# Kernel tuning notes

Hardware: AMD Instinct MI355X
Metric: run time of the kernel (lower is better)

Reference implementation:

```python
import jax, jax.numpy as jnp
import numpy as np

N_NODES = 50000
IN_DIM = 128
HIDDEN = 64
OUT_DIM = 3
HEADS1 = 4
NEG_SLOPE = 0.2
EPS = 1e-16


def _glorot(key, shape):
    fan_in, fan_out = shape[0], shape[-1]
    lim = (6.0 / (fan_in + fan_out)) ** 0.5
    return jax.random.uniform(key, shape, jnp.float32, -lim, lim)


def setup_inputs() -> dict:
    key = jax.random.key(0)
    ks = jax.random.split(key, 12)
    x = jax.random.normal(ks[0], (N_NODES, IN_DIM), jnp.float32)
    edge_index = jax.random.randint(ks[1], (2, 400000), 0, N_NODES, jnp.int64)
    # layer 1: GATConv(in=128, out=64, heads=4)
    W1 = _glorot(ks[2], (IN_DIM, HEADS1 * HIDDEN))
    att_src1 = _glorot(ks[3], (HEADS1, HIDDEN))
    att_dst1 = _glorot(ks[4], (HEADS1, HIDDEN))
    b1 = jnp.zeros((HEADS1 * HIDDEN,), jnp.float32)
    # layer 2: GATConv(in=256, out=64, heads=1)
    W2 = _glorot(ks[5], (HEADS1 * HIDDEN, HIDDEN))
    att_src2 = _glorot(ks[6], (1, HIDDEN))
    att_dst2 = _glorot(ks[7], (1, HIDDEN))
    b2 = jnp.zeros((HIDDEN,), jnp.float32)
    # output linear
    Wout = _glorot(ks[8], (HIDDEN, OUT_DIM))
    bout = jnp.zeros((OUT_DIM,), jnp.float32)
    return {"x": x, "edge_index": edge_index, "W1": W1, "att_src1": att_src1,
            "att_dst1": att_dst1, "b1": b1, "W2": W2, "att_src2": att_src2,
            "att_dst2": att_dst2, "b2": b2, "Wout": Wout, "bout": bout}


def gat_conv(x, src, dst, W, a_src, a_dst, b, n_nodes):
    H, C = a_src.shape
    h = (x @ W).reshape(n_nodes, H, C)            # [N,H,C]
    a_s = jnp.sum(h * a_src[None], axis=-1)        # [N,H]
    a_d = jnp.sum(h * a_dst[None], axis=-1)        # [N,H]
    e = jax.nn.leaky_relu(a_s[src] + a_d[dst], NEG_SLOPE)  # [E,H]
    # segment softmax over incoming edges of each dst node
    m = jax.ops.segment_max(e, dst, num_segments=n_nodes)
    ex = jnp.exp(e - m[dst])
    denom = jax.ops.segment_sum(ex, dst, num_segments=n_nodes)
    alpha = ex / (denom[dst] + EPS)                # [E,H]
    msg = h[src] * alpha[..., None]                # [E,H,C]
    out = jax.ops.segment_sum(msg, dst, num_segments=n_nodes)
    return out.reshape(n_nodes, H * C) + b


def reference(x, edge_index, W1, att_src1, att_dst1, b1, W2, att_src2, att_dst2, b2, Wout, bout):
    n = x.shape[0]
    loop = jnp.arange(n, dtype=edge_index.dtype)
    src = jnp.concatenate([edge_index[0], loop])   # add self loops (PyG default)
    dst = jnp.concatenate([edge_index[1], loop])
    h = gat_conv(x, src, dst, W1, att_src1, att_dst1, b1, n)
    h = jax.nn.elu(h)
    h = gat_conv(h, src, dst, W2, att_src2, att_dst2, b2, n)
    h = jax.nn.elu(h)
    return h @ Wout + bout
```

## Files before the change

kernel.cpp:

```cpp
#include <hip/hip_runtime.h>
#include <hip/hip_bf16.h>
#include <math.h>

#define N_NODES  50000
#define IN_DIM   128
#define HIDDEN   64
#define OUT_DIM  3
#define HEADS1   4
#define E_RAW    400000
#define E_TOT    450000
#define NEG_SLOPE 0.2f
#define SCAN_CHUNK 1024
#define N_CHUNKS ((N_NODES + SCAN_CHUNK - 1) / SCAN_CHUNK)
#define WPREP_BLOCKS 128

typedef __attribute__((ext_vector_type(8))) short bf16x8;
typedef __attribute__((ext_vector_type(4))) float f32x4;

static __device__ __forceinline__ float bfu(unsigned short u) {
    return __uint_as_float(((unsigned)u) << 16);
}
static __device__ __forceinline__ unsigned short f2b_bits(float v) {
    __hip_bfloat16 b = __float2bfloat16(v);
    return *reinterpret_cast<unsigned short*>(&b);
}

static __device__ __forceinline__ void get_edge(const int* __restrict__ ei, int is64,
                                                int e, int& s, int& d) {
    if (e >= E_RAW) { s = d = e - E_RAW; return; }
    if (is64) { s = ei[2 * e]; d = ei[2 * E_RAW + 2 * e]; }
    else      { s = ei[e];     d = ei[E_RAW + e]; }
    s = min(max(s, 0), N_NODES - 1);
    d = min(max(d, 0), N_NODES - 1);
}

__global__ void detect_zero_kernel(const int* __restrict__ ei, int* __restrict__ flag,
                                   int* __restrict__ deg) {
    int gid = blockIdx.x * 256 + threadIdx.x;
    for (int i = gid; i < N_NODES; i += 64 * 256) deg[i] = 0;
    if (blockIdx.x == 0) {
        int nz = 0;
        #pragma unroll 4
        for (int t = 0; t < 32; t++) {
            int i = t * 256 + threadIdx.x;
            nz |= ei[2 * i + 1];
        }
        __shared__ int s;
        if (threadIdx.x == 0) s = 0;
        __syncthreads();
        if (__any(nz != 0) && (threadIdx.x & 63) == 0) s = 1;
        __syncthreads();
        if (threadIdx.x == 0) flag[0] = s ? 0 : 1;
    }
}

__global__ void wprep_count_kernel(const float* __restrict__ W1, __hip_bfloat16* __restrict__ W1T,
                                   const float* __restrict__ W2, __hip_bfloat16* __restrict__ W2T,
                                   const int* __restrict__ ei, const int* __restrict__ flag,
                                   int* __restrict__ deg) {
    int bid = blockIdx.x;
    if (bid < WPREP_BLOCKS) {
        int i = bid * 256 + threadIdx.x;
        if (i < 256 * 128) {
            int n = i >> 7, k = i & 127;
            *((unsigned short*)W1T + i) = f2b_bits(W1[k * 256 + n]);
        }
        if (i < 64 * 256) {
            int n = i >> 8, k = i & 255;
            *((unsigned short*)W2T + i) = f2b_bits(W2[k * 64 + n]);
        }
        return;
    }
    int e = (bid - WPREP_BLOCKS) * 256 + threadIdx.x;
    if (e >= E_TOT) return;
    int s, d;
    get_edge(ei, flag[0], e, s, d);
    atomicAdd(&deg[d], 1);
}

__global__ void scan_local_kernel(const int* __restrict__ deg, int* __restrict__ row_ptr,
                                  int* __restrict__ bsums) {
    __shared__ int wsum[4];
    int t = threadIdx.x;
    int wv = t >> 6, ln = t & 63;
    int g = blockIdx.x * 256 + t;
    int4 d = (g < 12500) ? ((const int4*)deg)[g] : make_int4(0, 0, 0, 0);
    int p0 = d.x, p1 = p0 + d.y, p2 = p1 + d.z, p3 = p2 + d.w;
    int s = p3;
    #pragma unroll
    for (int off = 1; off < 64; off <<= 1) {
        int u = __shfl_up(s, off, 64);
        if (ln >= off) s += u;
    }
    if (ln == 63) wsum[wv] = s;
    __syncthreads();
    int wbase = 0;
    #pragma unroll
    for (int w = 0; w < 4; w++) wbase += (w < wv) ? wsum[w] : 0;
    int ex = wbase + s - p3;
    if (g < 12500) {
        int i = g * 4;
        row_ptr[i + 1] = ex + p0;
        row_ptr[i + 2] = ex + p1;
        row_ptr[i + 3] = ex + p2;
        row_ptr[i + 4] = ex + p3;
    }
    if (t == 255) bsums[blockIdx.x] = wbase + s;
    if (blockIdx.x == 0 && t == 0) row_ptr[0] = 0;
}

__global__ void scan_add_kernel(int* __restrict__ row_ptr, const int* __restrict__ bsums,
                                const int* __restrict__ deg, int* __restrict__ cursor) {
    __shared__ int soff[64];
    if (threadIdx.x < 64) {
        int v = (threadIdx.x < N_CHUNKS) ? bsums[threadIdx.x] : 0;
        #pragma unroll
        for (int off = 1; off < 64; off <<= 1) {
            int t = __shfl_up(v, off, 64);
            if (threadIdx.x >= off) v += t;
        }
        soff[threadIdx.x] = v;
    }
    __syncthreads();
    int i = blockIdx.x * blockDim.x + threadIdx.x;
    if (i < N_NODES) {
        int ch = i / SCAN_CHUNK;
        int add = (ch == 0) ? 0 : soff[ch - 1];
        int incl = row_ptr[i + 1] + add;
        row_ptr[i + 1] = incl;
        cursor[i] = incl - deg[i];
    }
}

__global__ void scatter_kernel(const int* __restrict__ ei, const int* __restrict__ flag,
                               int* __restrict__ cursor, int* __restrict__ csr_src) {
    int e = blockIdx.x * blockDim.x + threadIdx.x;
    if (e >= E_TOT) return;
    int s, d;
    get_edge(ei, flag[0], e, s, d);
    int pos = atomicAdd(&cursor[d], 1);
    csr_src[pos] = s;
}

__global__ void __launch_bounds__(256) gemm_l1_mfma_kernel(
        const float* __restrict__ x, const __hip_bfloat16* __restrict__ W1T,
        const float* __restrict__ att_s, const float* __restrict__ att_d,
        __hip_bfloat16* __restrict__ h1,
        float* __restrict__ asb4, float* __restrict__ adb4) {
    __shared__ unsigned short As[16][136];
    const int tid = threadIdx.x;
    const int wave = tid >> 6, lane = tid & 63;
    const int quad = lane >> 4, m = lane & 15;
    const int row0 = blockIdx.x * 16;
    {
        int r = tid >> 4, seg = tid & 15;
        const float* xa = x + (size_t)(row0 + r) * IN_DIM + seg * 8;
        float4 u = *(const float4*)xa;
        float4 v = *(const float4*)(xa + 4);
        ushort4 p0, p1;
        p0.x = f2b_bits(u.x); p0.y = f2b_bits(u.y); p0.z = f2b_bits(u.z); p0.w = f2b_bits(u.w);
        p1.x = f2b_bits(v.x); p1.y = f2b_bits(v.y); p1.z = f2b_bits(v.z); p1.w = f2b_bits(v.w);
        *(ushort4*)&As[r][seg * 8]     = p0;
        *(ushort4*)&As[r][seg * 8 + 4] = p1;
    }
    __syncthreads();
    const int n0w = wave * 64;
    f32x4 acc0 = {0.f, 0.f, 0.f, 0.f}, acc1 = acc0, acc2 = acc0, acc3 = acc0;
    #pragma unroll
    for (int k0 = 0; k0 < IN_DIM; k0 += 32) {
        int kk = k0 + quad * 8;
        bf16x8 a = *(const bf16x8*)&As[m][kk];
        bf16x8 b0 = *(const bf16x8*)(W1T + (size_t)(n0w +  0 + m) * IN_DIM + kk);
        bf16x8 b1 = *(const bf16x8*)(W1T + (size_t)(n0w + 16 + m) * IN_DIM + kk);
        bf16x8 b2 = *(const bf16x8*)(W1T + (size_t)(n0w + 32 + m) * IN_DIM + kk);
        bf16x8 b3 = *(const bf16x8*)(W1T + (size_t)(n0w + 48 + m) * IN_DIM + kk);
        acc0 = __builtin_amdgcn_mfma_f32_16x16x32_bf16(a, b0, acc0, 0, 0, 0);
        acc1 = __builtin_amdgcn_mfma_f32_16x16x32_bf16(a, b1, acc1, 0, 0, 0);
        acc2 = __builtin_amdgcn_mfma_f32_16x16x32_bf16(a, b2, acc2, 0, 0, 0);
        acc3 = __builtin_amdgcn_mfma_f32_16x16x32_bf16(a, b3, acc3, 0, 0, 0);
    }
    float ats0 = att_s[n0w +  0 + m], atd0 = att_d[n0w +  0 + m];
    float ats1 = att_s[n0w + 16 + m], atd1 = att_d[n0w + 16 + m];
    float ats2 = att_s[n0w + 32 + m], atd2 = att_d[n0w + 32 + m];
    float ats3 = att_s[n0w + 48 + m], atd3 = att_d[n0w + 48 + m];
    unsigned short* out = (unsigned short*)h1;
    #pragma unroll
    for (int i = 0; i < 4; i++) {
        int grow = row0 + quad * 4 + i;
        size_t base = (size_t)grow * 256;
        out[base + n0w +  0 + m] = f2b_bits(acc0[i]);
        out[base + n0w + 16 + m] = f2b_bits(acc1[i]);
        out[base + n0w + 32 + m] = f2b_bits(acc2[i]);
        out[base + n0w + 48 + m] = f2b_bits(acc3[i]);
        float ps = acc0[i] * ats0 + acc1[i] * ats1 + acc2[i] * ats2 + acc3[i] * ats3;
        float pd = acc0[i] * atd0 + acc1[i] * atd1 + acc2[i] * atd2 + acc3[i] * atd3;
        #pragma unroll
        for (int off = 1; off < 16; off <<= 1) {
            ps += __shfl_xor(ps, off, 16);
            pd += __shfl_xor(pd, off, 16);
        }
        if (m == 0) {
            asb4[grow * 4 + wave] = ps;
            adb4[grow * 4 + wave] = pd;
        }
    }
}

__global__ void __launch_bounds__(1024, 8) gat_gather4_l2_kernel(
        const int* __restrict__ row_ptr, const int* __restrict__ csr_src,
        const float* __restrict__ asb4, const float* __restrict__ adb4,
        const __hip_bfloat16* __restrict__ h1, const float* __restrict__ bias,
        const __hip_bfloat16* __restrict__ W2T,
        const float* __restrict__ att_s, const float* __restrict__ att_d,
        __hip_bfloat16* __restrict__ h2,
        float* __restrict__ asb, float* __restrict__ adb) {
    __shared__ unsigned short As[16][264];
    __shared__ float sPS[4][16];
    __shared__ float sPD[4][16];
    const int tid = threadIdx.x;
    const int wave = tid >> 6, lane = tid & 63;
    const int row0 = blockIdx.x * 16;
    const int c    = lane & 31;
    const int slot = lane >> 5;
    const int head = c >> 3;
    const int eidx0 = lane >> 2;
    const int hh   = lane & 3;

    {
        const int n = row0 + wave;
        int b = row_ptr[n], e = row_ptr[n + 1];
        float adnh = adb4[n * 4 + hh];
        float acc[8];
        #pragma unroll
        for (int i = 0; i < 8; i++) acc[i] = 0.f;
        float l = 0.f;
        for (int c0 = b; c0 < e; c0 += 16) {
            int cnt = min(16, e - c0);
            int s_all = (lane < cnt) ? csr_src[c0 + lane] : 0;
            int sE = __shfl(s_all, eidx0, 64);
            float w_all = 0.f;
            if (eidx0 < cnt) {
                float v = asb4[sE * 4 + hh] + adnh;
                v = (v > 0.f) ? v : NEG_SLOPE * v;
                w_all = __expf(v);
            }
            #pragma unroll 2
            for (int k = 0; k < cnt; k += 2) {
                int eidx = k + slot;
                int s = __shfl(s_all, eidx, 64);
                float w = __shfl(w_all, eidx * 4 + head, 64);
                bf16x8 f = *(const bf16x8*)(h1 + (size_t)s * 256 + c * 8);
                l += w;
                #pragma unroll
                for (int i = 0; i < 8; i++)
                    acc[i] += w * bfu((unsigned short)f[i]);
            }
        }
        #pragma unroll
        for (int i = 0; i < 8; i++) acc[i] += __shfl_xor(acc[i], 32, 64);
        l += __shfl_xor(l, 32, 64);
        if (lane < 32) {
            float il = 1.f / (l + 1e-16f);
            float4 b0 = *(const float4*)(bias + c * 8);
            float4 b1 = *(const float4*)(bias + c * 8 + 4);
            float r[8];
            r[0] = acc[0] * il + b0.x; r[1] = acc[1] * il + b0.y;
            r[2] = acc[2] * il + b0.z; r[3] = acc[3] * il + b0.w;
            r[4] = acc[4] * il + b1.x; r[5] = acc[5] * il + b1.y;
            r[6] = acc[6] * il + b1.z; r[7] = acc[7] * il + b1.w;
            bf16x8 st;
            #pragma unroll
            for (int i = 0; i < 8; i++) {
                float v = (r[i] > 0.f) ? r[i] : expm1f(r[i]);
                st[i] = (short)f2b_bits(v);
            }
            *(bf16x8*)&As[wave][c * 8] = st;
        }
    }
    __syncthreads();

    if (wave < 4) {
        const int quad = lane >> 4, m = lane & 15;
        const int n0 = wave * 16;
        f32x4 acc = {0.f, 0.f, 0.f, 0.f};
        #pragma unroll
        for (int k0 = 0; k0 < 256; k0 += 32) {
            int kk = k0 + quad * 8;
            bf16x8 a = *(const bf16x8*)&As[m][kk];
            bf16x8 bfr = *(const bf16x8*)(W2T + (size_t)(n0 + m) * 256 + kk);
            acc = __builtin_amdgcn_mfma_f32_16x16x32_bf16(a, bfr, acc, 0, 0, 0);
        }
        float ats = att_s[n0 + m], atd = att_d[n0 + m];
        unsigned short* out = (unsigned short*)h2;
        #pragma unroll
        for (int i = 0; i < 4; i++) {
            int grow = row0 + quad * 4 + i;
            out[(size_t)grow * 64 + n0 + m] = f2b_bits(acc[i]);
            float ps = acc[i] * ats;
            float pd = acc[i] * atd;
            #pragma unroll
            for (int off = 1; off < 16; off <<= 1) {
                ps += __shfl_xor(ps, off, 16);
                pd += __shfl_xor(pd, off, 16);
            }
            if (m == 0) {
                sPS[wave][quad * 4 + i] = ps;
                sPD[wave][quad * 4 + i] = pd;
            }
        }
    }
    __syncthreads();
    if (tid < 16) {
        float ps = sPS[0][tid] + sPS[1][tid] + sPS[2][tid] + sPS[3][tid];
        float pd = sPD[0][tid] + sPD[1][tid] + sPD[2][tid] + sPD[3][tid];
        asb[row0 + tid] = ps;
        adb[row0 + tid] = pd;
    }
}

__global__ void __launch_bounds__(256) gat_gather1_out_kernel(
        const int* __restrict__ row_ptr, const int* __restrict__ csr_src,
        const float* __restrict__ asb, const float* __restrict__ adb,
        const __hip_bfloat16* __restrict__ h2, const float* __restrict__ bias,
        const float* __restrict__ Wout, const float* __restrict__ bout,
        float* __restrict__ out) {
    int wave = threadIdx.x >> 6;
    int lane = threadIdx.x & 63;
    int n = blockIdx.x * 4 + wave;
    if (n >= N_NODES) return;
    int b = row_ptr[n], e = row_ptr[n + 1];
    const int c    = lane & 7;
    const int slot = lane >> 3;
    float adn = adb[n];
    float acc[8];
    #pragma unroll
    for (int i = 0; i < 8; i++) acc[i] = 0.f;
    float l = 0.f;
    for (int c0 = b; c0 < e; c0 += 64) {
        int cnt = min(64, e - c0);
        int s_all = (lane < cnt) ? csr_src[c0 + lane] : 0;
        float w_all = 0.f;
        if (lane < cnt) {
            float v = asb[s_all] + adn;
            v = (v > 0.f) ? v : NEG_SLOPE * v;
            w_all = __expf(v);
        }
        #pragma unroll 2
        for (int k = 0; k < cnt; k += 8) {
            int eidx = k + slot;
            int s = __shfl(s_all, eidx, 64);
            float w = __shfl(w_all, eidx, 64);
            bf16x8 f = *(const bf16x8*)(h2 + (size_t)s * 64 + c * 8);
            l += w;
            #pragma unroll
            for (int i = 0; i < 8; i++)
                acc[i] += w * bfu((unsigned short)f[i]);
        }
    }
    #pragma unroll
    for (int off = 8; off < 64; off <<= 1) {
        #pragma unroll
        for (int i = 0; i < 8; i++) acc[i] += __shfl_xor(acc[i], off, 64);
        l += __shfl_xor(l, off, 64);
    }
    float il = 1.f / (l + 1e-16f);
    float4 b0 = *(const float4*)(bias + c * 8);
    float4 b1 = *(const float4*)(bias + c * 8 + 4);
    float v[8];
    v[0] = acc[0] * il + b0.x; v[1] = acc[1] * il + b0.y;
    v[2] = acc[2] * il + b0.z; v[3] = acc[3] * il + b0.w;
    v[4] = acc[4] * il + b1.x; v[5] = acc[5] * il + b1.y;
    v[6] = acc[6] * il + b1.z; v[7] = acc[7] * il + b1.w;
    #pragma unroll
    for (int i = 0; i < 8; i++) v[i] = (v[i] > 0.f) ? v[i] : expm1f(v[i]);
    const float* wp = Wout + c * 24;
    float o0 = 0.f, o1 = 0.f, o2 = 0.f;
    #pragma unroll
    for (int i = 0; i < 8; i++) {
        o0 += v[i] * wp[i * 3 + 0];
        o1 += v[i] * wp[i * 3 + 1];
        o2 += v[i] * wp[i * 3 + 2];
    }
    #pragma unroll
    for (int off = 1; off < 8; off <<= 1) {
        o0 += __shfl_xor(o0, off, 64);
        o1 += __shfl_xor(o1, off, 64);
        o2 += __shfl_xor(o2, off, 64);
    }
    if (lane == 0) {
        out[n * OUT_DIM + 0] = o0 + bout[0];
        out[n * OUT_DIM + 1] = o1 + bout[1];
        out[n * OUT_DIM + 2] = o2 + bout[2];
    }
}

extern "C" void kernel_launch(void* const* d_in, const int* in_sizes, int n_in,
                              void* d_out, int out_size, void* d_ws, size_t ws_size,
                              hipStream_t stream) {
    const float* x    = (const float*)d_in[0];
    const int*   ei   = (const int*)d_in[1];
    const float* W1   = (const float*)d_in[2];
    const float* as1  = (const float*)d_in[3];
    const float* ad1  = (const float*)d_in[4];
    const float* b1   = (const float*)d_in[5];
    const float* W2   = (const float*)d_in[6];
    const float* as2  = (const float*)d_in[7];
    const float* ad2  = (const float*)d_in[8];
    const float* b2v  = (const float*)d_in[9];
    const float* Wout = (const float*)d_in[10];
    const float* bout = (const float*)d_in[11];
    float* out = (float*)d_out;

    float* ws    = (float*)d_ws;
    int*   flag  = (int*)ws;
    float* asb4  = ws + 16;
    float* adb4  = asb4 + (size_t)N_NODES * 4;
    float* asb1  = adb4 + (size_t)N_NODES * 4;
    float* adb1  = asb1 + N_NODES;
    __hip_bfloat16* h1     = (__hip_bfloat16*)(adb1 + N_NODES);
    __hip_bfloat16* h2     = (__hip_bfloat16*)(h1 + (size_t)N_NODES * 256);
    __hip_bfloat16* W1T    = (__hip_bfloat16*)(h2 + (size_t)N_NODES * 64);
    __hip_bfloat16* W2T    = W1T + 256 * 128;
    int* deg     = (int*)(W2T + 64 * 256);
    int* bsums   = deg + N_NODES;
    int* row_ptr = bsums + 64;
    int* cursor  = row_ptr + N_NODES + 16;
    int* csr_src = cursor + N_NODES;

    const int EB = (E_TOT + 255) / 256;
    const int NB = (N_NODES + 255) / 256;
    const int AB = (N_NODES + 3) / 4;
    const int MB = N_NODES / 16;

    detect_zero_kernel<<<64, 256, 0, stream>>>(ei, flag, deg);
    wprep_count_kernel<<<WPREP_BLOCKS + EB, 256, 0, stream>>>(W1, W1T, W2, W2T, ei, flag, deg);
    scan_local_kernel<<<N_CHUNKS, 256, 0, stream>>>(deg, row_ptr, bsums);
    scan_add_kernel<<<NB, 256, 0, stream>>>(row_ptr, bsums, deg, cursor);
    scatter_kernel<<<EB, 256, 0, stream>>>(ei, flag, cursor, csr_src);

    gemm_l1_mfma_kernel<<<MB, 256, 0, stream>>>(x, W1T, as1, ad1, h1, asb4, adb4);

    gat_gather4_l2_kernel<<<MB, 1024, 0, stream>>>(row_ptr, csr_src, asb4, adb4, h1, b1,
                                                   W2T, as2, ad2, h2, asb1, adb1);

    gat_gather1_out_kernel<<<AB, 256, 0, stream>>>(row_ptr, csr_src, asb1, adb1, h2,
                                                   b2v, Wout, bout, out);
}
```

Measured before the change: 263.9 us.

## Merge CSR scatter into layer-1 GEMM launch and shrink layer-2 gather blocks

The edge scatter into CSR and the layer-1 MFMA GEMM are combined into one launch. The first block range does the atomic scatter and the remaining blocks do the GEMM, so the two independent stages can overlap and one launch is removed. The layer-2 gather+GEMM kernel now uses 256-thread blocks covering 4 nodes instead of 1024-thread blocks covering 16. This gives finer-grained scheduling and less barrier stalling on uneven node degrees. In exchange, each 16-row MFMA tile now carries only 4 valid rows, so GEMM work per output row grows and W2T is re-read by four times as many blocks.

New measurement: 279.6 us. 1.06x slower.

```diff
diff --git a/kernel.cpp b/kernel.cpp
--- a/kernel.cpp
+++ b/kernel.cpp
@@ -13,6 +13,8 @@
 #define SCAN_CHUNK 1024
 #define N_CHUNKS ((N_NODES + SCAN_CHUNK - 1) / SCAN_CHUNK)
 #define WPREP_BLOCKS 128
+#define EB_SC ((E_TOT + 255) / 256)
+#define MB_GE (N_NODES / 16)
 
 typedef __attribute__((ext_vector_type(8))) short bf16x8;
 typedef __attribute__((ext_vector_type(4))) float f32x4;
@@ -132,26 +134,27 @@
     }
 }
 
-__global__ void scatter_kernel(const int* __restrict__ ei, const int* __restrict__ flag,
-                               int* __restrict__ cursor, int* __restrict__ csr_src) {
-    int e = blockIdx.x * blockDim.x + threadIdx.x;
-    if (e >= E_TOT) return;
-    int s, d;
-    get_edge(ei, flag[0], e, s, d);
-    int pos = atomicAdd(&cursor[d], 1);
-    csr_src[pos] = s;
-}
-
-__global__ void __launch_bounds__(256) gemm_l1_mfma_kernel(
+__global__ void __launch_bounds__(256) scatter_gemm_l1_kernel(
+        const int* __restrict__ ei, const int* __restrict__ flag,
+        int* __restrict__ cursor, int* __restrict__ csr_src,
         const float* __restrict__ x, const __hip_bfloat16* __restrict__ W1T,
         const float* __restrict__ att_s, const float* __restrict__ att_d,
         __hip_bfloat16* __restrict__ h1,
         float* __restrict__ asb4, float* __restrict__ adb4) {
     __shared__ unsigned short As[16][136];
+    if (blockIdx.x < EB_SC) {
+        int e = blockIdx.x * 256 + threadIdx.x;
+        if (e >= E_TOT) return;
+        int s, d;
+        get_edge(ei, flag[0], e, s, d);
+        int pos = atomicAdd(&cursor[d], 1);
+        csr_src[pos] = s;
+        return;
+    }
     const int tid = threadIdx.x;
     const int wave = tid >> 6, lane = tid & 63;
     const int quad = lane >> 4, m = lane & 15;
-    const int row0 = blockIdx.x * 16;
+    const int row0 = (blockIdx.x - EB_SC) * 16;
     {
         int r = tid >> 4, seg = tid & 15;
         const float* xa = x + (size_t)(row0 + r) * IN_DIM + seg * 8;
@@ -206,7 +209,7 @@
     }
 }
 
-__global__ void __launch_bounds__(1024, 8) gat_gather4_l2_kernel(
+__global__ void __launch_bounds__(256) gat_gather4_l2_kernel(
         const int* __restrict__ row_ptr, const int* __restrict__ csr_src,
         const float* __restrict__ asb4, const float* __restrict__ adb4,
         const __hip_bfloat16* __restrict__ h1, const float* __restrict__ bias,
@@ -215,11 +218,11 @@
         __hip_bfloat16* __restrict__ h2,
         float* __restrict__ asb, float* __restrict__ adb) {
     __shared__ unsigned short As[16][264];
-    __shared__ float sPS[4][16];
-    __shared__ float sPD[4][16];
+    __shared__ float sPS[4][4];
+    __shared__ float sPD[4][4];
     const int tid = threadIdx.x;
     const int wave = tid >> 6, lane = tid & 63;
-    const int row0 = blockIdx.x * 16;
+    const int row0 = blockIdx.x * 4;
     const int c    = lane & 31;
     const int slot = lane >> 5;
     const int head = c >> 3;
@@ -279,7 +282,7 @@
     }
     __syncthreads();
 
-    if (wave < 4) {
+    {
         const int quad = lane >> 4, m = lane & 15;
         const int n0 = wave * 16;
         f32x4 acc = {0.f, 0.f, 0.f, 0.f};
@@ -290,27 +293,29 @@
             bf16x8 bfr = *(const bf16x8*)(W2T + (size_t)(n0 + m) * 256 + kk);
             acc = __builtin_amdgcn_mfma_f32_16x16x32_bf16(a, bfr, acc, 0, 0, 0);
         }
-        float ats = att_s[n0 + m], atd = att_d[n0 + m];
-        unsigned short* out = (unsigned short*)h2;
-        #pragma unroll
-        for (int i = 0; i < 4; i++) {
-            int grow = row0 + quad * 4 + i;
-            out[(size_t)grow * 64 + n0 + m] = f2b_bits(acc[i]);
-            float ps = acc[i] * ats;
-            float pd = acc[i] * atd;
+        if (quad == 0) {
+            float ats = att_s[n0 + m], atd = att_d[n0 + m];
+            unsigned short* out = (unsigned short*)h2;
             #pragma unroll
-            for (int off = 1; off < 16; off <<= 1) {
-                ps += __shfl_xor(ps, off, 16);
-                pd += __shfl_xor(pd, off, 16);
+            for (int i = 0; i < 4; i++) {
+                int grow = row0 + i;
+                out[(size_t)grow * 64 + n0 + m] = f2b_bits(acc[i]);
+                float ps = acc[i] * ats;
+                float pd = acc[i] * atd;
+                #pragma unroll
+                for (int off = 1; off < 16; off <<= 1) {
+                    ps += __shfl_xor(ps, off, 16);
+                    pd += __shfl_xor(pd, off, 16);
+                }
+                if (m == 0) {
+                    sPS[wave][i] = ps;
+                    sPD[wave][i] = pd;
+                }
             }
-            if (m == 0) {
-                sPS[wave][quad * 4 + i] = ps;
-                sPD[wave][quad * 4 + i] = pd;
-            }
         }
     }
     __syncthreads();
-    if (tid < 16) {
+    if (tid < 4) {
         float ps = sPS[0][tid] + sPS[1][tid] + sPS[2][tid] + sPS[3][tid];
         float pd = sPD[0][tid] + sPD[1][tid] + sPD[2][tid] + sPD[3][tid];
         asb[row0 + tid] = ps;
@@ -427,21 +432,20 @@
     int* cursor  = row_ptr + N_NODES + 16;
     int* csr_src = cursor + N_NODES;
 
-    const int EB = (E_TOT + 255) / 256;
+    const int EB = EB_SC;
     const int NB = (N_NODES + 255) / 256;
     const int AB = (N_NODES + 3) / 4;
-    const int MB = N_NODES / 16;
 
     detect_zero_kernel<<<64, 256, 0, stream>>>(ei, flag, deg);
     wprep_count_kernel<<<WPREP_BLOCKS + EB, 256, 0, stream>>>(W1, W1T, W2, W2T, ei, flag, deg);
     scan_local_kernel<<<N_CHUNKS, 256, 0, stream>>>(deg, row_ptr, bsums);
     scan_add_kernel<<<NB, 256, 0, stream>>>(row_ptr, bsums, deg, cursor);
-    scatter_kernel<<<EB, 256, 0, stream>>>(ei, flag, cursor, csr_src);
-
-    gemm_l1_mfma_kernel<<<MB, 256, 0, stream>>>(x, W1T, as1, ad1, h1, asb4, adb4);
-
-    gat_gather4_l2_kernel<<<MB, 1024, 0, stream>>>(row_ptr, csr_src, asb4, adb4, h1, b1,
-                                                   W2T, as2, ad2, h2, asb1, adb1);
+
+    scatter_gemm_l1_kernel<<<EB + MB_GE, 256, 0, stream>>>(ei, flag, cursor, csr_src,
+                                                           x, W1T, as1, ad1, h1, asb4, adb4);
+
+    gat_gather4_l2_kernel<<<AB, 256, 0, stream>>>(row_ptr, csr_src, asb4, adb4, h1, b1,
+                                                  W2T, as2, ad2, h2, asb1, adb1);
 
     gat_gather1_out_kernel<<<AB, 256, 0, stream>>>(row_ptr, csr_src, asb1, adb1, h2,
                                                    b2v, Wout, bout, out);
```
